# Kernel optimization log

Measured on AMD Instinct MI355X. Metric: run time of the kernel, lower is better.

The kernel has to match this reference:

```python
import jax, jax.numpy as jnp
import numpy as np

B = 131072
PAD, SENS, HID = 3, 61, 64
NSTEPS = 10          # fixed dopri5 macro-steps over [0, TDELTA]
TDELTA = 1.0


def setup_inputs() -> dict:
    key = jax.random.key(0)
    ks = jax.random.split(key, 6)
    # xavier_uniform-ish (gain 0.5) small weights for stable dynamics
    def xav(k, fan_in, fan_out):
        lim = 0.5 * np.sqrt(6.0 / (fan_in + fan_out))
        return jax.random.uniform(k, (fan_in, fan_out), jnp.float32, -lim, lim)
    return {
        "pad_0": jax.random.normal(ks[0], (B, PAD), jnp.float32),
        "sensory": jax.random.normal(ks[1], (B, SENS), jnp.float32),
        "W1": xav(ks[2], PAD + SENS + 1, HID),
        "b1": jnp.zeros((HID,), jnp.float32),
        "W2": xav(ks[3], HID, HID),
        "b2": jnp.zeros((HID,), jnp.float32),
        "W3": xav(ks[4], HID, PAD),
        "b3": jnp.zeros((PAD,), jnp.float32),
        "scale": jnp.asarray(0.5, jnp.float32),
    }


def reference(pad_0, sensory, W1, b1, W2, b2, W3, b3, scale):
    """Integrate dPAD/dt = scale * tanh-MLP([pad, sensory, t]) from t=0 to TDELTA
    with fixed-step dopri5 (RK45) stages; returns final PAD state [B, 3]."""
    h = TDELTA / NSTEPS

    def f(t, y):
        tcol = jnp.full((y.shape[0], 1), t, dtype=y.dtype)
        x = jnp.concatenate([y, sensory, tcol], axis=-1)      # [B, 65]
        a = jnp.tanh(x @ W1 + b1)                             # [B, 64]
        a = jnp.tanh(a @ W2 + b2)                             # [B, 64]
        return jnp.tanh(a @ W3 + b3) * scale                  # [B, 3]

    def step(y, t0):
        # Dormand-Prince 5(4) stages; 5th-order solution weights
        k1 = f(t0, y)
        k2 = f(t0 + h / 5, y + h * (k1 / 5))
        k3 = f(t0 + 3 * h / 10, y + h * (3 / 40 * k1 + 9 / 40 * k2))
        k4 = f(t0 + 4 * h / 5, y + h * (44 / 45 * k1 - 56 / 15 * k2 + 32 / 9 * k3))
        k5 = f(t0 + 8 * h / 9, y + h * (19372 / 6561 * k1 - 25360 / 2187 * k2
                                        + 64448 / 6561 * k3 - 212 / 729 * k4))
        k6 = f(t0 + h, y + h * (9017 / 3168 * k1 - 355 / 33 * k2 + 46732 / 5247 * k3
                                + 49 / 176 * k4 - 5103 / 18656 * k5))
        y_new = y + h * (35 / 384 * k1 + 500 / 1113 * k3 + 125 / 192 * k4
                         - 2187 / 6784 * k5 + 11 / 84 * k6)
        return y_new, None

    ts = jnp.arange(NSTEPS, dtype=pad_0.dtype) * h
    y_final, _ = jax.lax.scan(jax.checkpoint(step), pad_0, ts)
    return y_final
```

## Files before the change

kernel.cpp:

```cpp
#include <hip/hip_runtime.h>

typedef __bf16 v8bf __attribute__((ext_vector_type(8)));
typedef float  v4f  __attribute__((ext_vector_type(4)));
typedef int    v4i  __attribute__((ext_vector_type(4)));
union FR { v4i i4; v8bf bf; };

static constexpr int BATCH = 131072;
static constexpr int SENSN = 61;
static constexpr int NSTEP = 10;
static constexpr int TPB   = 256;
static constexpr int ROWP  = 72;

#if __has_builtin(__builtin_amdgcn_exp2f)
#define EXP2(x) __builtin_amdgcn_exp2f(x)
#else
#define EXP2(x) exp2f(x)
#endif
#define RCP(x) __builtin_amdgcn_rcpf(x)

#define R64(M) \
  M(0) M(1) M(2) M(3) M(4) M(5) M(6) M(7) \
  M(8) M(9) M(10) M(11) M(12) M(13) M(14) M(15) \
  M(16) M(17) M(18) M(19) M(20) M(21) M(22) M(23) \
  M(24) M(25) M(26) M(27) M(28) M(29) M(30) M(31) \
  M(32) M(33) M(34) M(35) M(36) M(37) M(38) M(39) \
  M(40) M(41) M(42) M(43) M(44) M(45) M(46) M(47) \
  M(48) M(49) M(50) M(51) M(52) M(53) M(54) M(55) \
  M(56) M(57) M(58) M(59) M(60) M(61) M(62) M(63)

#define R32P(M) \
  M(0,1) M(2,3) M(4,5) M(6,7) M(8,9) M(10,11) M(12,13) M(14,15) \
  M(16,17) M(18,19) M(20,21) M(22,23) M(24,25) M(26,27) M(28,29) M(30,31) \
  M(32,33) M(34,35) M(36,37) M(38,39) M(40,41) M(42,43) M(44,45) M(46,47) \
  M(48,49) M(50,51) M(52,53) M(54,55) M(56,57) M(58,59) M(60,61) M(62,63)

__device__ __forceinline__ unsigned pk(float hi, float lo) {
    return __builtin_amdgcn_perm(__float_as_uint(hi), __float_as_uint(lo), 0x07060302u);
}

__global__ void __launch_bounds__(TPB, 2)
node_kernel(const float* __restrict__ pad0,
            const float* __restrict__ sens,
            const float* __restrict__ W1,
            const float* __restrict__ b1v,
            const float* __restrict__ W2,
            const float* __restrict__ b2v,
            const float* __restrict__ W3,
            const float* __restrict__ b3v,
            const float* __restrict__ scale_p,
            float* __restrict__ out)
{
    __shared__ ushort abuf[4 * 64 * ROWP];

    const int tid  = threadIdx.x;
    const int wv   = tid >> 6;
    const int lane = tid & 63;
    const int lo   = lane & 15;
    const int hh   = lane >> 4;
    const int b    = blockIdx.x * TPB + tid;

    ushort* __restrict__ aw = abuf + wv * 64 * ROWP;
    float*  __restrict__ ob = reinterpret_cast<float*>(aw);

    const float L     = 2.885390081777927f;
    const float scale = scale_p[0];
    const float m2L   = -2.0f * L;
    const float m2s   = -2.0f * scale;
    const float h     = 0.1f;

    FR b2f[4][2];
#pragma unroll
    for (int jb = 0; jb < 4; ++jb)
#pragma unroll
        for (int kc = 0; kc < 2; ++kc) {
            float w[8];
#pragma unroll
            for (int i = 0; i < 8; ++i)
                w[i] = W2[(hh*8 + i + 32*kc)*64 + lo + 16*jb];
            b2f[jb][kc].i4 = (v4i){ (int)pk(w[1],w[0]), (int)pk(w[3],w[2]),
                                    (int)pk(w[5],w[4]), (int)pk(w[7],w[6]) };
        }
    float W3L[4][4][3];
#pragma unroll
    for (int jb = 0; jb < 4; ++jb)
#pragma unroll
        for (int q = 0; q < 4; ++q)
#pragma unroll
            for (int n = 0; n < 3; ++n)
                W3L[jb][q][n] = W3[(16*jb + 4*hh + q)*3 + n];
    float b2c[4][4];
#pragma unroll
    for (int jb = 0; jb < 4; ++jb)
#pragma unroll
        for (int q = 0; q < 4; ++q)
            b2c[jb][q] = L * b2v[16*jb + 4*hh + q];
    const float b3L0 = L * b3v[0], b3L1 = L * b3v[1], b3L2 = L * b3v[2];

    const float* __restrict__ w1r0 = W1;
    const float* __restrict__ w1r1 = W1 + 64;
    const float* __restrict__ w1r2 = W1 + 128;
    const float* __restrict__ w1rt = W1 + 4096;

#define SDECL(j) float s_##j = b1v[j];
    R64(SDECL)
#undef SDECL
    {
        const float* __restrict__ srow = sens + (long)b * SENSN;
#pragma unroll 1
        for (int s = 0; s < SENSN; ++s) {
            const float xv = srow[s];
            const float* __restrict__ w = W1 + (3 + s) * 64;
#define SFMA(j) s_##j = fmaf(xv, w[j], s_##j);
            R64(SFMA)
#undef SFMA
        }
    }
#define SSC(j) s_##j *= L;
    R64(SSC)
#undef SSC

    float y0 = pad0[b*3 + 0];
    float y1 = pad0[b*3 + 1];
    float y2 = pad0[b*3 + 2];

    float k00=0,k01=0,k02=0, k10=0,k11=0,k12=0, k20=0,k21=0,k22=0,
          k30=0,k31=0,k32=0, k40=0,k41=0,k42=0;

#pragma unroll 1
    for (int step = 0; step < NSTEP; ++step) {
        const float t0 = (float)step * h;
#pragma unroll 1
        for (int st = 0; st < 6; ++st) {
            float tt = t0, v0 = y0, v1 = y1, v2 = y2;
            switch (st) {
            case 0: break;
            case 1: {
                const float a21 = 0.2f;
                v0 = fmaf(h, a21*k00, y0); v1 = fmaf(h, a21*k01, y1); v2 = fmaf(h, a21*k02, y2);
                tt = t0 + 0.2f*h;
            } break;
            case 2: {
                const float a31 = 3.f/40.f, a32 = 9.f/40.f;
                v0 = fmaf(h, a31*k00 + a32*k10, y0);
                v1 = fmaf(h, a31*k01 + a32*k11, y1);
                v2 = fmaf(h, a31*k02 + a32*k12, y2);
                tt = t0 + 0.3f*h;
            } break;
            case 3: {
                const float a41 = 44.f/45.f, a42 = -56.f/15.f, a43 = 32.f/9.f;
                v0 = fmaf(h, a41*k00 + a42*k10 + a43*k20, y0);
                v1 = fmaf(h, a41*k01 + a42*k11 + a43*k21, y1);
                v2 = fmaf(h, a41*k02 + a42*k12 + a43*k22, y2);
                tt = t0 + 0.8f*h;
            } break;
            case 4: {
                const float a51 = 19372.f/6561.f, a52 = -25360.f/2187.f,
                            a53 = 64448.f/6561.f, a54 = -212.f/729.f;
                v0 = fmaf(h, a51*k00 + a52*k10 + a53*k20 + a54*k30, y0);
                v1 = fmaf(h, a51*k01 + a52*k11 + a53*k21 + a54*k31, y1);
                v2 = fmaf(h, a51*k02 + a52*k12 + a53*k22 + a54*k32, y2);
                tt = t0 + (8.f/9.f)*h;
            } break;
            default: {
                const float a61 = 9017.f/3168.f, a62 = -355.f/33.f,
                            a63 = 46732.f/5247.f, a64 = 49.f/176.f, a65 = -5103.f/18656.f;
                v0 = fmaf(h, a61*k00 + a62*k10 + a63*k20 + a64*k30 + a65*k40, y0);
                v1 = fmaf(h, a61*k01 + a62*k11 + a63*k21 + a64*k31 + a65*k41, y1);
                v2 = fmaf(h, a61*k02 + a62*k12 + a63*k22 + a64*k32 + a65*k42, y2);
                tt = t0 + h;
            } break;
            }
            const float v0p = L*v0, v1p = L*v1, v2p = L*v2, ttp = L*tt;

            unsigned pw[32];
#define L1P(i0,i1) { \
    float za = s_##i0; \
    za = fmaf(v0p, w1r0[i0], za); za = fmaf(v1p, w1r1[i0], za); \
    za = fmaf(v2p, w1r2[i0], za); za = fmaf(ttp, w1rt[i0], za); \
    float ta = fmaf(m2L, RCP(EXP2(za) + 1.0f), L); \
    float zb = s_##i1; \
    zb = fmaf(v0p, w1r0[i1], zb); zb = fmaf(v1p, w1r1[i1], zb); \
    zb = fmaf(v2p, w1r2[i1], zb); zb = fmaf(ttp, w1rt[i1], zb); \
    float tb = fmaf(m2L, RCP(EXP2(zb) + 1.0f), L); \
    pw[(i0)/2] = pk(tb, ta); }
            R32P(L1P)
#undef L1P
            {
                v4i* __restrict__ dst = (v4i*)&aw[lane * ROWP];
#pragma unroll
                for (int w8 = 0; w8 < 8; ++w8)
                    dst[w8] = (v4i){ (int)pw[4*w8+0], (int)pw[4*w8+1],
                                     (int)pw[4*w8+2], (int)pw[4*w8+3] };
            }
            asm volatile("" ::: "memory");

            const v4f z4 = {0.f, 0.f, 0.f, 0.f};
            v4f acc[4][4];
#pragma unroll
            for (int nb = 0; nb < 4; ++nb) {
                FR a0, a1;
                a0.i4 = *(const v4i*)&aw[(lo + 16*nb)*ROWP + hh*8];
                a1.i4 = *(const v4i*)&aw[(lo + 16*nb)*ROWP + hh*8 + 32];
#pragma unroll
                for (int jb = 0; jb < 4; ++jb) {
                    v4f t = __builtin_amdgcn_mfma_f32_16x16x32_bf16(b2f[jb][0].bf, a0.bf, z4, 0, 0, 0);
                    acc[jb][nb] = __builtin_amdgcn_mfma_f32_16x16x32_bf16(b2f[jb][1].bf, a1.bf, t, 0, 0, 0);
                }
            }

#pragma unroll
            for (int jb = 0; jb < 4; ++jb)
#pragma unroll
                for (int nb = 0; nb < 4; ++nb)
#pragma unroll
                    for (int q = 0; q < 4; ++q) {
                        float z = acc[jb][nb][q] + b2c[jb][q];
                        acc[jb][nb][q] = fmaf(m2L, RCP(EXP2(z) + 1.0f), L);
                    }

            float p[4][3];
#pragma unroll
            for (int nb = 0; nb < 4; ++nb)
#pragma unroll
                for (int n = 0; n < 3; ++n) {
                    float s = 0.0f;
#pragma unroll
                    for (int jb = 0; jb < 4; ++jb)
#pragma unroll
                        for (int q = 0; q < 4; ++q)
                            s = fmaf(acc[jb][nb][q], W3L[jb][q][n], s);
                    p[nb][n] = s;
                }
#pragma unroll
            for (int nb = 0; nb < 4; ++nb)
#pragma unroll
                for (int n = 0; n < 3; ++n) {
                    float v = p[nb][n];
                    v += __shfl_xor(v, 16, 64);
                    v += __shfl_xor(v, 32, 64);
                    p[nb][n] = v;
                }

            if (hh == 0) {
#pragma unroll
                for (int nb = 0; nb < 4; ++nb)
#pragma unroll
                    for (int n = 0; n < 3; ++n)
                        ob[(lo + 16*nb)*4 + n] = p[nb][n];
            }
            asm volatile("" ::: "memory");

            const float4 ov = *(const float4*)&ob[lane * 4];
            const float r0 = fmaf(m2s, RCP(EXP2(ov.x + b3L0) + 1.0f), scale);
            const float r1 = fmaf(m2s, RCP(EXP2(ov.y + b3L1) + 1.0f), scale);
            const float r2 = fmaf(m2s, RCP(EXP2(ov.z + b3L2) + 1.0f), scale);
            asm volatile("" ::: "memory");

            switch (st) {
            case 0: k00=r0; k01=r1; k02=r2; break;
            case 1: k10=r0; k11=r1; k12=r2; break;
            case 2: k20=r0; k21=r1; k22=r2; break;
            case 3: k30=r0; k31=r1; k32=r2; break;
            case 4: k40=r0; k41=r1; k42=r2; break;
            default: {
                const float c1 = 35.f/384.f,  c3c = 500.f/1113.f,
                            c4 = 125.f/192.f, c5 = -2187.f/6784.f, c6 = 11.f/84.f;
                y0 = fmaf(h, c1*k00 + c3c*k20 + c4*k30 + c5*k40 + c6*r0, y0);
                y1 = fmaf(h, c1*k01 + c3c*k21 + c4*k31 + c5*k41 + c6*r1, y1);
                y2 = fmaf(h, c1*k02 + c3c*k22 + c4*k32 + c5*k42 + c6*r2, y2);
            } break;
            }
        }
    }

    out[b*3 + 0] = y0;
    out[b*3 + 1] = y1;
    out[b*3 + 2] = y2;
}

extern "C" void kernel_launch(void* const* d_in, const int* in_sizes, int n_in,
                              void* d_out, int out_size, void* d_ws, size_t ws_size,
                              hipStream_t stream) {
    const float* pad0 = (const float*)d_in[0];
    const float* sens = (const float*)d_in[1];
    const float* W1   = (const float*)d_in[2];
    const float* b1v  = (const float*)d_in[3];
    const float* W2   = (const float*)d_in[4];
    const float* b2v  = (const float*)d_in[5];
    const float* W3   = (const float*)d_in[6];
    const float* b3v  = (const float*)d_in[7];
    const float* sc   = (const float*)d_in[8];
    float* outp = (float*)d_out;

    dim3 grid(BATCH / TPB), block(TPB);
    hipLaunchKernelGGL(node_kernel, grid, block, 0, stream,
                       pad0, sens, W1, b1v, W2, b2v, W3, b3v, sc, outp);
}
```

Measured before the change: 574.2 us.

## Fuse layer-2 tanh into W3 dot products and reduce outputs via butterfly shuffles

Applies the layer-2 tanh per 16-row block straight after its MFMAs and accumulates the W3 projection at once, so the 4x4 array of accumulators no longer stays live. The 24 xor-shuffles plus the LDS store/load of the three outputs are replaced by a transpose-style butterfly of 9 shuffles, which leaves each lane with its own row's outputs. The LDS row pitch also goes from 72 to 96 elements, and launch bounds become explicit flat-work-group/waves-per-EU attributes. The new padding enlarges LDS use and may change the bank-conflict pattern of the row-wise fragment loads.

```diff
diff --git a/kernel.cpp b/kernel.cpp
--- a/kernel.cpp
+++ b/kernel.cpp
@@ -9,7 +9,7 @@
 static constexpr int SENSN = 61;
 static constexpr int NSTEP = 10;
 static constexpr int TPB   = 256;
-static constexpr int ROWP  = 72;
+static constexpr int ROWP  = 96;
 
 #if __has_builtin(__builtin_amdgcn_exp2f)
 #define EXP2(x) __builtin_amdgcn_exp2f(x)
@@ -38,7 +38,8 @@
     return __builtin_amdgcn_perm(__float_as_uint(hi), __float_as_uint(lo), 0x07060302u);
 }
 
-__global__ void __launch_bounds__(TPB, 2)
+__global__ void
+__attribute__((amdgpu_flat_work_group_size(256, 256), amdgpu_waves_per_eu(2, 2)))
 node_kernel(const float* __restrict__ pad0,
             const float* __restrict__ sens,
             const float* __restrict__ W1,
@@ -57,10 +58,11 @@
     const int lane = tid & 63;
     const int lo   = lane & 15;
     const int hh   = lane >> 4;
+    const int hh0  = (lane >> 4) & 1;
+    const int hh1  = (lane >> 5) & 1;
     const int b    = blockIdx.x * TPB + tid;
 
     ushort* __restrict__ aw = abuf + wv * 64 * ROWP;
-    float*  __restrict__ ob = reinterpret_cast<float*>(aw);
 
     const float L     = 2.885390081777927f;
     const float scale = scale_p[0];
@@ -195,66 +197,58 @@
             asm volatile("" ::: "memory");
 
             const v4f z4 = {0.f, 0.f, 0.f, 0.f};
-            v4f acc[4][4];
+            float p[4][3];
+#pragma unroll
+            for (int nb = 0; nb < 4; ++nb) { p[nb][0]=0.f; p[nb][1]=0.f; p[nb][2]=0.f; }
 #pragma unroll
             for (int nb = 0; nb < 4; ++nb) {
                 FR a0, a1;
                 a0.i4 = *(const v4i*)&aw[(lo + 16*nb)*ROWP + hh*8];
                 a1.i4 = *(const v4i*)&aw[(lo + 16*nb)*ROWP + hh*8 + 32];
+                v4f acc[4];
 #pragma unroll
                 for (int jb = 0; jb < 4; ++jb) {
                     v4f t = __builtin_amdgcn_mfma_f32_16x16x32_bf16(b2f[jb][0].bf, a0.bf, z4, 0, 0, 0);
-                    acc[jb][nb] = __builtin_amdgcn_mfma_f32_16x16x32_bf16(b2f[jb][1].bf, a1.bf, t, 0, 0, 0);
+                    acc[jb] = __builtin_amdgcn_mfma_f32_16x16x32_bf16(b2f[jb][1].bf, a1.bf, t, 0, 0, 0);
                 }
-            }
-
-#pragma unroll
-            for (int jb = 0; jb < 4; ++jb)
-#pragma unroll
-                for (int nb = 0; nb < 4; ++nb)
+#pragma unroll
+                for (int jb = 0; jb < 4; ++jb)
 #pragma unroll
                     for (int q = 0; q < 4; ++q) {
-                        float z = acc[jb][nb][q] + b2c[jb][q];
-                        acc[jb][nb][q] = fmaf(m2L, RCP(EXP2(z) + 1.0f), L);
+                        float z  = acc[jb][q] + b2c[jb][q];
+                        float t2 = fmaf(m2L, RCP(EXP2(z) + 1.0f), L);
+                        p[nb][0] = fmaf(t2, W3L[jb][q][0], p[nb][0]);
+                        p[nb][1] = fmaf(t2, W3L[jb][q][1], p[nb][1]);
+                        p[nb][2] = fmaf(t2, W3L[jb][q][2], p[nb][2]);
                     }
-
-            float p[4][3];
-#pragma unroll
-            for (int nb = 0; nb < 4; ++nb)
+            }
+            asm volatile("" ::: "memory");
+
+            float q2[2][3];
+#pragma unroll
+            for (int j2 = 0; j2 < 2; ++j2)
 #pragma unroll
                 for (int n = 0; n < 3; ++n) {
-                    float s = 0.0f;
-#pragma unroll
-                    for (int jb = 0; jb < 4; ++jb)
-#pragma unroll
-                        for (int q = 0; q < 4; ++q)
-                            s = fmaf(acc[jb][nb][q], W3L[jb][q][n], s);
-                    p[nb][n] = s;
+                    float keep = hh1 ? p[2+j2][n] : p[j2][n];
+                    float send = hh1 ? p[j2][n]   : p[2+j2][n];
+                    q2[j2][n] = keep + __shfl_xor(send, 32, 64);
                 }
-#pragma unroll
-            for (int nb = 0; nb < 4; ++nb)
-#pragma unroll
-                for (int n = 0; n < 3; ++n) {
-                    float v = p[nb][n];
-                    v += __shfl_xor(v, 16, 64);
-                    v += __shfl_xor(v, 32, 64);
-                    p[nb][n] = v;
-                }
-
-            if (hh == 0) {
-#pragma unroll
-                for (int nb = 0; nb < 4; ++nb)
-#pragma unroll
-                    for (int n = 0; n < 3; ++n)
-                        ob[(lo + 16*nb)*4 + n] = p[nb][n];
-            }
-            asm volatile("" ::: "memory");
-
-            const float4 ov = *(const float4*)&ob[lane * 4];
-            const float r0 = fmaf(m2s, RCP(EXP2(ov.x + b3L0) + 1.0f), scale);
-            const float r1 = fmaf(m2s, RCP(EXP2(ov.y + b3L1) + 1.0f), scale);
-            const float r2 = fmaf(m2s, RCP(EXP2(ov.z + b3L2) + 1.0f), scale);
-            asm volatile("" ::: "memory");
+            float o0, o1, o2;
+            {
+                float keep0 = hh0 ? q2[1][0] : q2[0][0];
+                float send0 = hh0 ? q2[0][0] : q2[1][0];
+                o0 = keep0 + __shfl_xor(send0, 16, 64);
+                float keep1 = hh0 ? q2[1][1] : q2[0][1];
+                float send1 = hh0 ? q2[0][1] : q2[1][1];
+                o1 = keep1 + __shfl_xor(send1, 16, 64);
+                float keep2 = hh0 ? q2[1][2] : q2[0][2];
+                float send2 = hh0 ? q2[0][2] : q2[1][2];
+                o2 = keep2 + __shfl_xor(send2, 16, 64);
+            }
+
+            const float r0 = fmaf(m2s, RCP(EXP2(o0 + b3L0) + 1.0f), scale);
+            const float r1 = fmaf(m2s, RCP(EXP2(o1 + b3L1) + 1.0f), scale);
+            const float r2 = fmaf(m2s, RCP(EXP2(o2 + b3L2) + 1.0f), scale);
 
             switch (st) {
             case 0: k00=r0; k01=r1; k02=r2; break;
```

Measured after the change: 501.6 us. -12.7%, faster.
